# Kernel tuning notes

Hardware: AMD Instinct MI355X
Metric: run time of the kernel (lower is better)

Reference implementation:

```python
import jax, jax.numpy as jnp
import numpy as np

H = 16      # num_heads
D = 64      # head_dim
SCALE = (2 * D) ** -0.5


def setup_inputs() -> dict:
    key = jax.random.key(0)
    k1, k2, k3, k4, k5 = jax.random.split(key, 5)
    tokens = jax.random.normal(k1, (4, 2048, 1024), dtype=jnp.float32)
    sen = jax.random.normal(k2, (4, 1, 1024), dtype=jnp.float32)
    W1 = jax.random.normal(k3, (1024, 3072), dtype=jnp.float32) * (1024 ** -0.5)
    W2 = jax.random.normal(k4, (1024, 2048), dtype=jnp.float32) * (1024 ** -0.5)
    mask = jax.random.randint(k5, (4, 2048), 0, 2, dtype=jnp.int32)
    return {"tokens": tokens, "sen": sen, "W1": W1, "W2": W2, "mask": mask}


def _split_heads(t):
    # [b, n, h*d] -> [b, h, n, d]
    b, n, _ = t.shape
    return t.reshape(b, n, H, D).transpose(0, 2, 1, 3)


def reference(tokens, sen, W1, W2, mask):
    b, n, _ = tokens.shape
    # token-stream qkv: [b, n, 3*h*d]
    q1, k1, v1 = (_split_heads(t) for t in jnp.split(tokens @ W1, 3, axis=-1))
    # sentence-stream qk: sen has seq len 1 -> [b, h, 1, d]
    q2, k2 = (_split_heads(t) for t in jnp.split(sen @ W2, 2, axis=-1))
    # dual-source scores: [b,h,n,n] + broadcast [b,h,1,1]
    dots = SCALE * (jnp.einsum('bhnd,bhmd->bhnm', q1, k1)
                    + jnp.einsum('bhnd,bhmd->bhnm', q2, k2))
    m = mask[:, None, None, :].astype(dots.dtype)
    dots = dots - 10000.0 * (1.0 - m)
    attn = jax.nn.softmax(dots, axis=-1)
    out = jnp.einsum('bhnm,bhmd->bhnd', attn, v1)
    return out.transpose(0, 2, 1, 3).reshape(b, n, H * D)
```

## Files before the change

kernel.cpp:

```cpp
#include <hip/hip_runtime.h>
#include <cstdint>


typedef __bf16 bf16x8 __attribute__((ext_vector_type(8)));
typedef __bf16 bf16x4 __attribute__((ext_vector_type(4)));
typedef float  f32x4  __attribute__((ext_vector_type(4)));

#define MFMA16(a, b, c) __builtin_amdgcn_mfma_f32_16x16x32_bf16(a, b, c, 0, 0, 0)

__device__ __forceinline__ float exp2_raw(float x) {
    float r; asm("v_exp_f32 %0, %1" : "=v"(r) : "v"(x)); return r;
}
__device__ __forceinline__ void lds_fence() {
    asm volatile("s_waitcnt lgkmcnt(0)" ::: "memory");
    __builtin_amdgcn_sched_barrier(0);
}

static constexpr float QSCALE = 0.12751879523486166f;

__global__ __launch_bounds__(256) void k_cvt_tok(const float* __restrict__ in,
                                                 __bf16* __restrict__ out) {
    int i = (blockIdx.x * 256 + threadIdx.x) * 4;
    float4 v = *(const float4*)&in[i];
    bf16x4 o = {(__bf16)v.x, (__bf16)v.y, (__bf16)v.z, (__bf16)v.w};
    *(bf16x4*)&out[i] = o;
}

__global__ __launch_bounds__(256) void k_w1t(const float* __restrict__ W1,
                                             __bf16* __restrict__ W1T) {
    __shared__ float t[32][33];
    int bx = blockIdx.x % 96, by = blockIdx.x / 96;
    int r0 = by * 32, c0 = bx * 32;
    int tr = threadIdx.x >> 3, tc = (threadIdx.x & 7) * 4;
    float4 v = *(const float4*)&W1[(size_t)(r0 + tr) * 3072 + c0 + tc];
    t[tr][tc + 0] = v.x; t[tr][tc + 1] = v.y; t[tr][tc + 2] = v.z; t[tr][tc + 3] = v.w;
    __syncthreads();
    bf16x4 o = {(__bf16)t[tc + 0][tr], (__bf16)t[tc + 1][tr],
                (__bf16)t[tc + 2][tr], (__bf16)t[tc + 3][tr]};
    *(bf16x4*)&W1T[(size_t)(c0 + tr) * 1024 + r0 + tc] = o;
}

__global__ __launch_bounds__(256) void k_mask(const int* __restrict__ m,
                                              __bf16* __restrict__ fl) {
    int i = blockIdx.x * 256 + threadIdx.x;
    fl[i] = (__bf16)(float)m[i];
}

__global__ __launch_bounds__(256) void k_gemm_qkv(const __bf16* __restrict__ A,
                                                  const __bf16* __restrict__ BT,
                                                  const __bf16* __restrict__ FLAG,
                                                  __bf16* __restrict__ Q,
                                                  __bf16* __restrict__ K,
                                                  __bf16* __restrict__ VT) {
    __shared__ __align__(16) __bf16 Asm[128 * 32];
    __shared__ __align__(16) __bf16 Bsm[128 * 32];
    const int tid = threadIdx.x;
    const int tm = blockIdx.x / 24, tn = blockIdx.x % 24;
    const int m0 = tm * 128, n0 = tn * 128;
    const int l = tid & 63, wv = tid >> 6;
    const int l15 = l & 15, l4 = l >> 4;
    const int wr = wv >> 1, wc = wv & 1;

    const size_t aoff = (size_t)(m0 + wv * 32 + (l >> 2)) * 2048 + (l & 3) * 16;
    const size_t boff = (size_t)(n0 + wv * 32 + (l >> 2)) * 2048 + (l & 3) * 16;
    const char* Ab = (const char*)A;
    const char* Bb = (const char*)BT;
    char* asml = (char*)Asm + wv * 2048;
    char* bsml = (char*)Bsm + wv * 2048;

    f32x4 acc[4][4];
#pragma unroll
    for (int i = 0; i < 4; ++i)
#pragma unroll
        for (int j = 0; j < 4; ++j) acc[i][j] = (f32x4){0.f, 0.f, 0.f, 0.f};

    for (int kt = 0; kt < 32; ++kt) {
        __syncthreads();
#pragma unroll
        for (int i = 0; i < 2; ++i) {
            __builtin_amdgcn_global_load_lds(
                (const __attribute__((address_space(1))) void*)(Ab + aoff + (size_t)i * 32768 + (size_t)kt * 64),
                (__attribute__((address_space(3))) void*)(asml + i * 1024), 16, 0, 0);
            __builtin_amdgcn_global_load_lds(
                (const __attribute__((address_space(1))) void*)(Bb + boff + (size_t)i * 32768 + (size_t)kt * 64),
                (__attribute__((address_space(3))) void*)(bsml + i * 1024), 16, 0, 0);
        }
        __syncthreads();

        bf16x8 af[4], bb[4];
#pragma unroll
        for (int mi = 0; mi < 4; ++mi)
            af[mi] = *(const bf16x8*)((const char*)Asm + (wr * 64 + mi * 16 + l15) * 64 + l4 * 16);
#pragma unroll
        for (int ni = 0; ni < 4; ++ni)
            bb[ni] = *(const bf16x8*)((const char*)Bsm + (wc * 64 + ni * 16 + l15) * 64 + l4 * 16);
#pragma unroll
        for (int mi = 0; mi < 4; ++mi)
#pragma unroll
            for (int ni = 0; ni < 4; ++ni)
                acc[mi][ni] = MFMA16(af[mi], bb[ni], acc[mi][ni]);
    }

#pragma unroll
    for (int mi = 0; mi < 4; ++mi) {
        const int rowb = m0 + wr * 64 + mi * 16 + l4 * 4;
        const int b = rowb >> 11, n = rowb & 2047;
#pragma unroll
        for (int ni = 0; ni < 4; ++ni) {
            const int col = n0 + wc * 64 + ni * 16 + l15;
            const int str = col >> 10, cc = col & 1023;
            const int h = cc >> 6, d = cc & 63;
            const int bh = b * 16 + h;
            if (str == 2) {
                const bf16x4 fl = *(const bf16x4*)&FLAG[b * 2048 + n];
                bf16x4 pv = {(__bf16)(acc[mi][ni][0] * (float)fl[0]),
                             (__bf16)(acc[mi][ni][1] * (float)fl[1]),
                             (__bf16)(acc[mi][ni][2] * (float)fl[2]),
                             (__bf16)(acc[mi][ni][3] * (float)fl[3])};
                *(bf16x4*)&VT[((size_t)bh * 64 + d) * 2048 + n] = pv;
            } else if (str == 0) {
#pragma unroll
                for (int r = 0; r < 4; ++r)
                    Q[((size_t)bh * 2048 + n + r) * 64 + d] = (__bf16)(acc[mi][ni][r] * QSCALE);
            } else {
#pragma unroll
                for (int r = 0; r < 4; ++r)
                    K[((size_t)bh * 2048 + n + r) * 64 + d] = (__bf16)acc[mi][ni][r];
            }
        }
    }
}

__global__ __launch_bounds__(256) void k_attn(const __bf16* __restrict__ Q,
                                              const __bf16* __restrict__ K,
                                              const __bf16* __restrict__ VT,
                                              const __bf16* __restrict__ FLAG,
                                              float* __restrict__ out) {
    __shared__ __align__(16) char smem[29952];
    __bf16* Ksm = (__bf16*)smem;
    __bf16* Vsm = (__bf16*)(smem + 9216);
    char*   Psw = smem + 20736;

    const int tid = threadIdx.x;
    const int bh = blockIdx.x >> 5, qt = blockIdx.x & 31;
    const int b = bh >> 4, h = bh & 15;
    const int wv = tid >> 6, l = tid & 63, l15 = l & 15, l4 = l >> 4;
    char* Pw = Psw + wv * 2304;

    const size_t qrow = (size_t)bh * 2048 + qt * 64 + wv * 16 + l15;
    const bf16x8 q0 = *(const bf16x8*)&Q[qrow * 64 + l4 * 8];
    const bf16x8 q1 = *(const bf16x8*)&Q[qrow * 64 + 32 + l4 * 8];

    float m_run = -1e30f;
    f32x4 o[4], o4;
#pragma unroll
    for (int i = 0; i < 4; ++i) o[i] = (f32x4){0.f, 0.f, 0.f, 0.f};
    o4 = (f32x4){0.f, 0.f, 0.f, 0.f};

    const char* Kg = (const char*)K + (size_t)bh * 2048 * 128;
    const char* Vg = (const char*)VT + (size_t)bh * 64 * 4096;
    const char* Fg = (const char*)FLAG + (size_t)b * 4096;

    for (int t = 0; t < 32; ++t) {
        __syncthreads();
#pragma unroll
        for (int i = 0; i < 2; ++i) {
            int c = tid * 2 + i;
            int row = c >> 3, qq = c & 7;
            *(uint4*)((char*)Ksm + row * 144 + qq * 16) =
                *(const uint4*)(Kg + (size_t)t * 8192 + c * 16);
            *(uint4*)((char*)Vsm + row * 144 + qq * 16) =
                *(const uint4*)(Vg + (size_t)row * 4096 + t * 128 + qq * 16);
        }
        if (tid < 8)
            *(uint4*)((char*)Vsm + 64 * 144 + tid * 16) = *(const uint4*)(Fg + t * 128 + tid * 16);
        __syncthreads();

        f32x4 s[4];
#pragma unroll
        for (int kb = 0; kb < 4; ++kb) {
            bf16x8 kf0 = *(const bf16x8*)((const char*)Ksm + (kb * 16 + l15) * 144 + l4 * 16);
            bf16x8 kf1 = *(const bf16x8*)((const char*)Ksm + (kb * 16 + l15) * 144 + 64 + l4 * 16);
            s[kb] = (f32x4){0.f, 0.f, 0.f, 0.f};
            s[kb] = MFMA16(kf0, q0, s[kb]);
            s[kb] = MFMA16(kf1, q1, s[kb]);
        }

        float mx = fmaxf(fmaxf(s[0][0], s[0][1]), fmaxf(s[0][2], s[0][3]));
#pragma unroll
        for (int kb = 1; kb < 4; ++kb)
            mx = fmaxf(mx, fmaxf(fmaxf(s[kb][0], s[kb][1]), fmaxf(s[kb][2], s[kb][3])));
        mx = fmaxf(mx, __shfl_xor(mx, 16, 64));
        mx = fmaxf(mx, __shfl_xor(mx, 32, 64));

        if (!__all(mx <= m_run + 8.0f)) {
            const float m_new = fmaxf(m_run, mx);
            const float al = exp2_raw(m_run - m_new);
#pragma unroll
            for (int db = 0; db < 4; ++db) o[db] *= al;
            o4 *= al;
            m_run = m_new;
        }

        bf16x4 pk[4];
#pragma unroll
        for (int kb = 0; kb < 4; ++kb)
#pragma unroll
            for (int r = 0; r < 4; ++r)
                pk[kb][r] = (__bf16)exp2_raw(s[kb][r] - m_run);

#pragma unroll
        for (int kb = 0; kb < 4; ++kb)
            *(bf16x4*)(Pw + l15 * 144 + kb * 32 + l4 * 8) = pk[kb];
        lds_fence();

        bf16x8 p0 = *(const bf16x8*)(Pw + l15 * 144 + l4 * 16);
        bf16x8 p1 = *(const bf16x8*)(Pw + l15 * 144 + 64 + l4 * 16);
#pragma unroll
        for (int db = 0; db < 4; ++db) {
            bf16x8 v0 = *(const bf16x8*)((const char*)Vsm + (db * 16 + l15) * 144 + l4 * 16);
            bf16x8 v1 = *(const bf16x8*)((const char*)Vsm + (db * 16 + l15) * 144 + 64 + l4 * 16);
            o[db] = MFMA16(v0, p0, o[db]);
            o[db] = MFMA16(v1, p1, o[db]);
        }
        {
            bf16x8 f0 = *(const bf16x8*)((const char*)Vsm + (64 + l15) * 144 + l4 * 16);
            bf16x8 f1 = *(const bf16x8*)((const char*)Vsm + (64 + l15) * 144 + 64 + l4 * 16);
            o4 = MFMA16(f0, p0, o4);
            o4 = MFMA16(f1, p1, o4);
        }
    }

    __syncthreads();
    const float denom = __shfl(o4[0], l15, 64);
    const float inv = 1.0f / denom;
    float* osm = (float*)smem + wv * 1040;
#pragma unroll
    for (int db = 0; db < 4; ++db)
#pragma unroll
        for (int r = 0; r < 4; ++r)
            osm[l15 * 65 + db * 16 + l4 * 4 + r] = o[db][r] * inv;
    lds_fence();
    const size_t nbase = (size_t)qt * 64 + wv * 16;
#pragma unroll
    for (int qi = 0; qi < 16; ++qi)
        out[((size_t)b * 2048 + nbase + qi) * 1024 + h * 64 + l] = osm[qi * 65 + l];
}

extern "C" void kernel_launch(void* const* d_in, const int* in_sizes, int n_in,
                              void* d_out, int out_size, void* d_ws, size_t ws_size,
                              hipStream_t stream) {
    const float* tokens = (const float*)d_in[0];
    const float* W1 = (const float*)d_in[2];
    const int* mask = (const int*)d_in[4];
    float* out = (float*)d_out;

    char* w = (char*)d_ws;
    __bf16* tokbf = (__bf16*)(w + 0);
    __bf16* w1t   = (__bf16*)(w + 16777216);
    __bf16* qarr  = (__bf16*)(w + 23068672);
    __bf16* karr  = (__bf16*)(w + 39845888);
    __bf16* vtar  = (__bf16*)(w + 56623104);
    __bf16* flagb = (__bf16*)(w + 73400320);

    k_cvt_tok<<<8192, 256, 0, stream>>>(tokens, tokbf);
    k_w1t<<<3072, 256, 0, stream>>>(W1, w1t);
    k_mask<<<32, 256, 0, stream>>>(mask, flagb);
    k_gemm_qkv<<<1536, 256, 0, stream>>>(tokbf, w1t, flagb, qarr, karr, vtar);
    k_attn<<<2048, 256, 0, stream>>>(qarr, karr, vtar, flagb, out);
}
```

Baseline: 322.1 us.

## Rework attention to 32x32 MFMA tiles with double-buffered LDS and swizzled grids

Measured after the change: 264.8 us. 1.22x faster.

```diff
diff --git a/kernel.cpp b/kernel.cpp
--- a/kernel.cpp
+++ b/kernel.cpp
@@ -5,16 +5,36 @@
 typedef __bf16 bf16x8 __attribute__((ext_vector_type(8)));
 typedef __bf16 bf16x4 __attribute__((ext_vector_type(4)));
 typedef float  f32x4  __attribute__((ext_vector_type(4)));
-
-#define MFMA16(a, b, c) __builtin_amdgcn_mfma_f32_16x16x32_bf16(a, b, c, 0, 0, 0)
-
-__device__ __forceinline__ float exp2_raw(float x) {
+typedef float  f32x16 __attribute__((ext_vector_type(16)));
+typedef unsigned int u32x4 __attribute__((ext_vector_type(4)));
+
+#define MFMA16(a,b,c) __builtin_amdgcn_mfma_f32_16x16x32_bf16(a,b,c,0,0,0)
+#define MFMA32(a,b,c) __builtin_amdgcn_mfma_f32_32x32x16_bf16(a,b,c,0,0,0)
+
+static __device__ __forceinline__ float exp2_raw(float x) {
     float r; asm("v_exp_f32 %0, %1" : "=v"(r) : "v"(x)); return r;
 }
-__device__ __forceinline__ void lds_fence() {
+static __device__ __forceinline__ uint32_t pkbf16(float a, float b) {
+    uint32_t r; asm("v_cvt_pk_bf16_f32 %0, %1, %2" : "=v"(r) : "v"(a), "v"(b)); return r;
+}
+static __device__ __forceinline__ void lds_fence() {
     asm volatile("s_waitcnt lgkmcnt(0)" ::: "memory");
     __builtin_amdgcn_sched_barrier(0);
 }
+static __device__ __forceinline__ f32x16 zero16() {
+    f32x16 z;
+#pragma unroll
+    for (int i = 0; i < 16; ++i) z[i] = 0.f;
+    return z;
+}
+static __device__ __forceinline__ bf16x8 zero8() {
+    return __builtin_bit_cast(bf16x8, (u32x4){0u, 0u, 0u, 0u});
+}
+
+#define GLLDS(src, dst)                                                        \
+    __builtin_amdgcn_global_load_lds(                                          \
+        (const __attribute__((address_space(1))) void*)(src),                  \
+        (__attribute__((address_space(3))) void*)(dst), 16, 0, 0)
 
 static constexpr float QSCALE = 0.12751879523486166f;
 
@@ -41,9 +61,13 @@
 }
 
 __global__ __launch_bounds__(256) void k_mask(const int* __restrict__ m,
-                                              __bf16* __restrict__ fl) {
+                                              __bf16* __restrict__ fl,
+                                              __bf16* __restrict__ flp) {
     int i = blockIdx.x * 256 + threadIdx.x;
     fl[i] = (__bf16)(float)m[i];
+    int s6 = i & 63;
+    int kp = ((s6 >> 2) & 1) * 32 + ((s6 >> 4) & 3) * 8 + ((s6 >> 3) & 1) * 4 + (s6 & 3);
+    flp[i] = (__bf16)(float)m[(i & ~63) | kp];
 }
 
 __global__ __launch_bounds__(256) void k_gemm_qkv(const __bf16* __restrict__ A,
@@ -52,21 +76,20 @@
                                                   __bf16* __restrict__ Q,
                                                   __bf16* __restrict__ K,
                                                   __bf16* __restrict__ VT) {
-    __shared__ __align__(16) __bf16 Asm[128 * 32];
-    __shared__ __align__(16) __bf16 Bsm[128 * 32];
+    __shared__ __align__(16) char gsm[32768];
     const int tid = threadIdx.x;
-    const int tm = blockIdx.x / 24, tn = blockIdx.x % 24;
+    const int bid = blockIdx.x;
+    const int sw = (bid & 7) * 192 + (bid >> 3);
+    const int tm = sw / 24, tn = sw % 24;
     const int m0 = tm * 128, n0 = tn * 128;
     const int l = tid & 63, wv = tid >> 6;
     const int l15 = l & 15, l4 = l >> 4;
     const int wr = wv >> 1, wc = wv & 1;
 
+    const char* Ab = (const char*)A;
+    const char* Bb = (const char*)BT;
     const size_t aoff = (size_t)(m0 + wv * 32 + (l >> 2)) * 2048 + (l & 3) * 16;
     const size_t boff = (size_t)(n0 + wv * 32 + (l >> 2)) * 2048 + (l & 3) * 16;
-    const char* Ab = (const char*)A;
-    const char* Bb = (const char*)BT;
-    char* asml = (char*)Asm + wv * 2048;
-    char* bsml = (char*)Bsm + wv * 2048;
 
     f32x4 acc[4][4];
 #pragma unroll
@@ -74,26 +97,31 @@
 #pragma unroll
         for (int j = 0; j < 4; ++j) acc[i][j] = (f32x4){0.f, 0.f, 0.f, 0.f};
 
+    auto STAGE = [&](int nb, int kt) {
+        char* ab = gsm + nb * 16384 + wv * 2048;
+        char* bb = ab + 8192;
+#pragma unroll
+        for (int i = 0; i < 2; ++i) {
+            GLLDS(Ab + aoff + (size_t)i * 32768 + (size_t)kt * 64, ab + i * 1024);
+            GLLDS(Bb + boff + (size_t)i * 32768 + (size_t)kt * 64, bb + i * 1024);
+        }
+    };
+    STAGE(0, 0);
+
     for (int kt = 0; kt < 32; ++kt) {
+        const int cur = kt & 1;
         __syncthreads();
-#pragma unroll
-        for (int i = 0; i < 2; ++i) {
-            __builtin_amdgcn_global_load_lds(
-                (const __attribute__((address_space(1))) void*)(Ab + aoff + (size_t)i * 32768 + (size_t)kt * 64),
-                (__attribute__((address_space(3))) void*)(asml + i * 1024), 16, 0, 0);
-            __builtin_amdgcn_global_load_lds(
-                (const __attribute__((address_space(1))) void*)(Bb + boff + (size_t)i * 32768 + (size_t)kt * 64),
-                (__attribute__((address_space(3))) void*)(bsml + i * 1024), 16, 0, 0);
-        }
-        __syncthreads();
+        if (kt < 31) STAGE(cur ^ 1, kt + 1);
+        const char* As = gsm + cur * 16384;
+        const char* Bs = As + 8192;
 
         bf16x8 af[4], bb[4];
 #pragma unroll
         for (int mi = 0; mi < 4; ++mi)
-            af[mi] = *(const bf16x8*)((const char*)Asm + (wr * 64 + mi * 16 + l15) * 64 + l4 * 16);
+            af[mi] = *(const bf16x8*)(As + (wr * 64 + mi * 16 + l15) * 64 + l4 * 16);
 #pragma unroll
         for (int ni = 0; ni < 4; ++ni)
-            bb[ni] = *(const bf16x8*)((const char*)Bsm + (wc * 64 + ni * 16 + l15) * 64 + l4 * 16);
+            bb[ni] = *(const bf16x8*)(Bs + (wc * 64 + ni * 16 + l15) * 64 + l4 * 16);
 #pragma unroll
         for (int mi = 0; mi < 4; ++mi)
 #pragma unroll
@@ -112,12 +140,15 @@
             const int h = cc >> 6, d = cc & 63;
             const int bh = b * 16 + h;
             if (str == 2) {
-                const bf16x4 fl = *(const bf16x4*)&FLAG[b * 2048 + n];
-                bf16x4 pv = {(__bf16)(acc[mi][ni][0] * (float)fl[0]),
-                             (__bf16)(acc[mi][ni][1] * (float)fl[1]),
-                             (__bf16)(acc[mi][ni][2] * (float)fl[2]),
-                             (__bf16)(acc[mi][ni][3] * (float)fl[3])};
-                *(bf16x4*)&VT[((size_t)bh * 64 + d) * 2048 + n] = pv;
+                const bf16x4 fv = *(const bf16x4*)&FLAG[b * 2048 + n];
+                bf16x4 pv = {(__bf16)(acc[mi][ni][0] * (float)fv[0]),
+                             (__bf16)(acc[mi][ni][1] * (float)fv[1]),
+                             (__bf16)(acc[mi][ni][2] * (float)fv[2]),
+                             (__bf16)(acc[mi][ni][3] * (float)fv[3])};
+                const int k6 = n & 63;
+                const int nsl = (n & ~63) | (((k6 >> 3) & 3) << 4) |
+                                (((k6 >> 2) & 1) << 3) | ((k6 >> 5) << 2);
+                *(bf16x4*)&VT[((size_t)bh * 64 + d) * 2048 + nsl] = pv;
             } else if (str == 0) {
 #pragma unroll
                 for (int r = 0; r < 4; ++r)
@@ -131,120 +162,168 @@
     }
 }
 
-__global__ __launch_bounds__(256) void k_attn(const __bf16* __restrict__ Q,
-                                              const __bf16* __restrict__ K,
-                                              const __bf16* __restrict__ VT,
-                                              const __bf16* __restrict__ FLAG,
-                                              float* __restrict__ out) {
-    __shared__ __align__(16) char smem[29952];
-    __bf16* Ksm = (__bf16*)smem;
-    __bf16* Vsm = (__bf16*)(smem + 9216);
-    char*   Psw = smem + 20736;
-
+__global__ __launch_bounds__(256, 2) void k_attn(const __bf16* __restrict__ Q,
+                                                 const __bf16* __restrict__ K,
+                                                 const __bf16* __restrict__ VT,
+                                                 const __bf16* __restrict__ FLAGP,
+                                                 float* __restrict__ out) {
+    __shared__ __align__(16) char smem[33280];
     const int tid = threadIdx.x;
-    const int bh = blockIdx.x >> 5, qt = blockIdx.x & 31;
+    const int bid = blockIdx.x;
+    const int swz = (bid & 7) * 64 + (bid >> 3);
+    const int bh = swz >> 3, qt = swz & 7;
     const int b = bh >> 4, h = bh & 15;
-    const int wv = tid >> 6, l = tid & 63, l15 = l & 15, l4 = l >> 4;
-    char* Pw = Psw + wv * 2304;
-
-    const size_t qrow = (size_t)bh * 2048 + qt * 64 + wv * 16 + l15;
-    const bf16x8 q0 = *(const bf16x8*)&Q[qrow * 64 + l4 * 8];
-    const bf16x8 q1 = *(const bf16x8*)&Q[qrow * 64 + 32 + l4 * 8];
-
-    float m_run = -1e30f;
-    f32x4 o[4], o4;
-#pragma unroll
-    for (int i = 0; i < 4; ++i) o[i] = (f32x4){0.f, 0.f, 0.f, 0.f};
-    o4 = (f32x4){0.f, 0.f, 0.f, 0.f};
+    const int wv = tid >> 6, l = tid & 63, l31 = l & 31, hi = l >> 5;
 
     const char* Kg = (const char*)K + (size_t)bh * 2048 * 128;
     const char* Vg = (const char*)VT + (size_t)bh * 64 * 4096;
-    const char* Fg = (const char*)FLAG + (size_t)b * 4096;
+    const __bf16* Fg = FLAGP + b * 2048;
+
+    const __bf16* qp = Q + ((size_t)bh * 2048 + qt * 256 + wv * 64 + l31) * 64;
+    bf16x8 qf0[4], qf1[4];
+#pragma unroll
+    for (int m = 0; m < 4; ++m) {
+        qf0[m] = *(const bf16x8*)(qp + m * 16 + hi * 8);
+        qf1[m] = *(const bf16x8*)(qp + 32 * 64 + m * 16 + hi * 8);
+    }
+
+    f32x16 o00 = zero16(), o01 = zero16(), o10 = zero16(), o11 = zero16();
+    f32x16 fa0 = zero16(), fa1 = zero16();
+    float mr0 = -1e30f, mr1 = -1e30f;
+
+    auto STAGE = [&](int nb, int t) {
+        char* base = smem + nb * 16384;
+#pragma unroll
+        for (int i = 0; i < 2; ++i) {
+            const int blk = wv + i * 4;
+            const int mc = blk >> 1, rb = blk & 1;
+            const int row = rb * 32 + (l >> 1);
+            GLLDS(Kg + (size_t)(t * 64 + row) * 128 + mc * 32 + (l & 1) * 16,
+                  base + blk * 1024);
+            GLLDS(Vg + (size_t)row * 4096 + t * 128 + mc * 32 + (l & 1) * 16,
+                  base + 8192 + blk * 1024);
+        }
+    };
+    STAGE(0, 0);
 
     for (int t = 0; t < 32; ++t) {
+        const int cur = t & 1;
         __syncthreads();
-#pragma unroll
-        for (int i = 0; i < 2; ++i) {
-            int c = tid * 2 + i;
-            int row = c >> 3, qq = c & 7;
-            *(uint4*)((char*)Ksm + row * 144 + qq * 16) =
-                *(const uint4*)(Kg + (size_t)t * 8192 + c * 16);
-            *(uint4*)((char*)Vsm + row * 144 + qq * 16) =
-                *(const uint4*)(Vg + (size_t)row * 4096 + t * 128 + qq * 16);
-        }
-        if (tid < 8)
-            *(uint4*)((char*)Vsm + 64 * 144 + tid * 16) = *(const uint4*)(Fg + t * 128 + tid * 16);
-        __syncthreads();
-
-        f32x4 s[4];
-#pragma unroll
-        for (int kb = 0; kb < 4; ++kb) {
-            bf16x8 kf0 = *(const bf16x8*)((const char*)Ksm + (kb * 16 + l15) * 144 + l4 * 16);
-            bf16x8 kf1 = *(const bf16x8*)((const char*)Ksm + (kb * 16 + l15) * 144 + 64 + l4 * 16);
-            s[kb] = (f32x4){0.f, 0.f, 0.f, 0.f};
-            s[kb] = MFMA16(kf0, q0, s[kb]);
-            s[kb] = MFMA16(kf1, q1, s[kb]);
-        }
-
-        float mx = fmaxf(fmaxf(s[0][0], s[0][1]), fmaxf(s[0][2], s[0][3]));
-#pragma unroll
-        for (int kb = 1; kb < 4; ++kb)
-            mx = fmaxf(mx, fmaxf(fmaxf(s[kb][0], s[kb][1]), fmaxf(s[kb][2], s[kb][3])));
-        mx = fmaxf(mx, __shfl_xor(mx, 16, 64));
-        mx = fmaxf(mx, __shfl_xor(mx, 32, 64));
-
-        if (!__all(mx <= m_run + 8.0f)) {
-            const float m_new = fmaxf(m_run, mx);
-            const float al = exp2_raw(m_run - m_new);
-#pragma unroll
-            for (int db = 0; db < 4; ++db) o[db] *= al;
-            o4 *= al;
-            m_run = m_new;
-        }
-
-        bf16x4 pk[4];
-#pragma unroll
-        for (int kb = 0; kb < 4; ++kb)
-#pragma unroll
-            for (int r = 0; r < 4; ++r)
-                pk[kb][r] = (__bf16)exp2_raw(s[kb][r] - m_run);
-
-#pragma unroll
-        for (int kb = 0; kb < 4; ++kb)
-            *(bf16x4*)(Pw + l15 * 144 + kb * 32 + l4 * 8) = pk[kb];
+        if (t < 31) STAGE(cur ^ 1, t + 1);
+        const char* Ks = smem + cur * 16384;
+        const char* Vs = Ks + 8192;
+
+        bf16x8 kf0[4], kf1[4];
+#pragma unroll
+        for (int m = 0; m < 4; ++m) {
+            kf0[m] = *(const bf16x8*)(Ks + m * 2048 + l31 * 32 + hi * 16);
+            kf1[m] = *(const bf16x8*)(Ks + m * 2048 + (32 + l31) * 32 + hi * 16);
+        }
+
+        f32x16 s0 = zero16(), s1 = zero16();
+#pragma unroll
+        for (int m = 0; m < 4; ++m) s0 = MFMA32(kf0[m], qf0[m], s0);
+#pragma unroll
+        for (int m = 0; m < 4; ++m) s1 = MFMA32(kf1[m], qf0[m], s1);
+        {
+            float mx = fmaxf(s0[0], s1[0]);
+#pragma unroll
+            for (int i = 1; i < 16; ++i) mx = fmaxf(mx, fmaxf(s0[i], s1[i]));
+            mx = fmaxf(mx, __shfl_xor(mx, 32, 64));
+            if (!__all(mx <= mr0 + 8.0f)) {
+                float mn = fmaxf(mr0, mx);
+                float al = exp2_raw(mr0 - mn);
+                o00 *= al; o01 *= al; fa0 *= al; mr0 = mn;
+            }
+        }
+        u32x4 pk0[4];
+#pragma unroll
+        for (int m = 0; m < 4; ++m) {
+            pk0[m].x = pkbf16(exp2_raw(s0[4 * m] - mr0), exp2_raw(s0[4 * m + 1] - mr0));
+            pk0[m].y = pkbf16(exp2_raw(s0[4 * m + 2] - mr0), exp2_raw(s0[4 * m + 3] - mr0));
+            pk0[m].z = pkbf16(exp2_raw(s1[4 * m] - mr0), exp2_raw(s1[4 * m + 1] - mr0));
+            pk0[m].w = pkbf16(exp2_raw(s1[4 * m + 2] - mr0), exp2_raw(s1[4 * m + 3] - mr0));
+        }
+
+        bf16x8 ff[4];
+#pragma unroll
+        for (int m = 0; m < 4; ++m) ff[m] = zero8();
+        if (l31 == 0) {
+#pragma unroll
+            for (int m = 0; m < 4; ++m)
+                ff[m] = *(const bf16x8*)(Fg + t * 64 + m * 16 + hi * 8);
+        }
+
+        s0 = zero16(); s1 = zero16();
+#pragma unroll
+        for (int m = 0; m < 4; ++m) s0 = MFMA32(kf0[m], qf1[m], s0);
+#pragma unroll
+        for (int m = 0; m < 4; ++m) s1 = MFMA32(kf1[m], qf1[m], s1);
+        {
+            float mx = fmaxf(s0[0], s1[0]);
+#pragma unroll
+            for (int i = 1; i < 16; ++i) mx = fmaxf(mx, fmaxf(s0[i], s1[i]));
+            mx = fmaxf(mx, __shfl_xor(mx, 32, 64));
+            if (!__all(mx <= mr1 + 8.0f)) {
+                float mn = fmaxf(mr1, mx);
+                float al = exp2_raw(mr1 - mn);
+                o10 *= al; o11 *= al; fa1 *= al; mr1 = mn;
+            }
+        }
+        u32x4 pk1[4];
+#pragma unroll
+        for (int m = 0; m < 4; ++m) {
+            pk1[m].x = pkbf16(exp2_raw(s0[4 * m] - mr1), exp2_raw(s0[4 * m + 1] - mr1));
+            pk1[m].y = pkbf16(exp2_raw(s0[4 * m + 2] - mr1), exp2_raw(s0[4 * m + 3] - mr1));
+            pk1[m].z = pkbf16(exp2_raw(s1[4 * m] - mr1), exp2_raw(s1[4 * m + 1] - mr1));
+            pk1[m].w = pkbf16(exp2_raw(s1[4 * m + 2] - mr1), exp2_raw(s1[4 * m + 3] - mr1));
+        }
+
+#pragma unroll
+        for (int m = 0; m < 4; ++m) {
+            bf16x8 vf0 = *(const bf16x8*)(Vs + m * 2048 + l31 * 32 + hi * 16);
+            bf16x8 vf1 = *(const bf16x8*)(Vs + m * 2048 + (32 + l31) * 32 + hi * 16);
+            bf16x8 p0 = __builtin_bit_cast(bf16x8, pk0[m]);
+            bf16x8 p1 = __builtin_bit_cast(bf16x8, pk1[m]);
+            o00 = MFMA32(vf0, p0, o00);
+            o01 = MFMA32(vf1, p0, o01);
+            o10 = MFMA32(vf0, p1, o10);
+            o11 = MFMA32(vf1, p1, o11);
+            fa0 = MFMA32(ff[m], p0, fa0);
+            fa1 = MFMA32(ff[m], p1, fa1);
+        }
+    }
+
+    __syncthreads();
+    float* osm = (float*)smem + wv * 2080;
+    const size_t obase = ((size_t)b * 2048 + qt * 256 + wv * 64) * 1024 + h * 64 + l;
+    {
+        const float inv = 1.0f / __shfl(fa0[0], l31, 64);
+#pragma unroll
+        for (int r = 0; r < 16; ++r) {
+            const int d = (r & 3) + 8 * (r >> 2) + 4 * hi;
+            osm[l31 * 65 + d] = o00[r] * inv;
+            osm[l31 * 65 + d + 32] = o01[r] * inv;
+        }
         lds_fence();
-
-        bf16x8 p0 = *(const bf16x8*)(Pw + l15 * 144 + l4 * 16);
-        bf16x8 p1 = *(const bf16x8*)(Pw + l15 * 144 + 64 + l4 * 16);
-#pragma unroll
-        for (int db = 0; db < 4; ++db) {
-            bf16x8 v0 = *(const bf16x8*)((const char*)Vsm + (db * 16 + l15) * 144 + l4 * 16);
-            bf16x8 v1 = *(const bf16x8*)((const char*)Vsm + (db * 16 + l15) * 144 + 64 + l4 * 16);
-            o[db] = MFMA16(v0, p0, o[db]);
-            o[db] = MFMA16(v1, p1, o[db]);
-        }
-        {
-            bf16x8 f0 = *(const bf16x8*)((const char*)Vsm + (64 + l15) * 144 + l4 * 16);
-            bf16x8 f1 = *(const bf16x8*)((const char*)Vsm + (64 + l15) * 144 + 64 + l4 * 16);
-            o4 = MFMA16(f0, p0, o4);
-            o4 = MFMA16(f1, p1, o4);
-        }
-    }
-
-    __syncthreads();
-    const float denom = __shfl(o4[0], l15, 64);
-    const float inv = 1.0f / denom;
-    float* osm = (float*)smem + wv * 1040;
-#pragma unroll
-    for (int db = 0; db < 4; ++db)
-#pragma unroll
-        for (int r = 0; r < 4; ++r)
-            osm[l15 * 65 + db * 16 + l4 * 4 + r] = o[db][r] * inv;
-    lds_fence();
-    const size_t nbase = (size_t)qt * 64 + wv * 16;
-#pragma unroll
-    for (int qi = 0; qi < 16; ++qi)
-        out[((size_t)b * 2048 + nbase + qi) * 1024 + h * 64 + l] = osm[qi * 65 + l];
+#pragma unroll
+        for (int qi = 0; qi < 32; ++qi)
+            out[obase + (size_t)qi * 1024] = osm[qi * 65 + l];
+        lds_fence();
+    }
+    {
+        const float inv = 1.0f / __shfl(fa1[0], l31, 64);
+#pragma unroll
+        for (int r = 0; r < 16; ++r) {
+            const int d = (r & 3) + 8 * (r >> 2) + 4 * hi;
+            osm[l31 * 65 + d] = o10[r] * inv;
+            osm[l31 * 65 + d + 32] = o11[r] * inv;
+        }
+        lds_fence();
+#pragma unroll
+        for (int qi = 0; qi < 32; ++qi)
+            out[obase + (size_t)(32 + qi) * 1024] = osm[qi * 65 + l];
+    }
 }
 
 extern "C" void kernel_launch(void* const* d_in, const int* in_sizes, int n_in,
@@ -262,10 +341,11 @@
     __bf16* karr  = (__bf16*)(w + 39845888);
     __bf16* vtar  = (__bf16*)(w + 56623104);
     __bf16* flagb = (__bf16*)(w + 73400320);
+    __bf16* flagp = (__bf16*)(w + 73416704);
 
     k_cvt_tok<<<8192, 256, 0, stream>>>(tokens, tokbf);
     k_w1t<<<3072, 256, 0, stream>>>(W1, w1t);
-    k_mask<<<32, 256, 0, stream>>>(mask, flagb);
+    k_mask<<<32, 256, 0, stream>>>(mask, flagb, flagp);
     k_gemm_qkv<<<1536, 256, 0, stream>>>(tokbf, w1t, flagb, qarr, karr, vtar);
-    k_attn<<<2048, 256, 0, stream>>>(qarr, karr, vtar, flagb, out);
-}
+    k_attn<<<512, 256, 0, stream>>>(qarr, karr, vtar, flagp, out);
+}
```
